# Optimization experiments

Measured on AMD Instinct MI355X. Metric: run time of the kernel, lower is better.

## Reference

```python
import jax, jax.numpy as jnp
import numpy as np

GRID_SIZE = 5
SPLINE_ORDER = 3
B = 524288


def make_grid(in_features, grid_size=GRID_SIZE, spline_order=SPLINE_ORDER, grid_range=(-1.0, 1.0)):
    h = (grid_range[1] - grid_range[0]) / grid_size
    g = jnp.arange(-spline_order, grid_size + spline_order + 1, dtype=jnp.float32) * h + grid_range[0]
    return jnp.tile(g[None, :], (in_features, 1))  # (in, grid_size + 2*order + 1)


def b_splines(x, grid, order=SPLINE_ORDER):
    # x: (B, in), grid: (in, G). Cox-de Boor recursion, matching efficient-kan.
    xe = x[:, :, None]  # (B, in, 1)
    g = grid[None, :, :]  # (1, in, G)
    bases = ((xe >= g[:, :, :-1]) & (xe < g[:, :, 1:])).astype(x.dtype)
    for k in range(1, order + 1):
        left = (xe - g[:, :, : -(k + 1)]) / (g[:, :, k:-1] - g[:, :, : -(k + 1)])
        right = (g[:, :, k + 1:] - xe) / (g[:, :, k + 1:] - g[:, :, 1:-k])
        bases = left * bases[:, :, :-1] + right * bases[:, :, 1:]
    return bases  # (B, in, grid_size + order)


def kan_linear(x, base_w, spline_w, scaler, grid):
    # base path: SiLU activation then dense
    base_out = jax.nn.silu(x) @ base_w.T  # (B, out)
    # spline path
    bs = b_splines(x, grid)  # (B, in, K)
    scaled_sw = spline_w * scaler[:, :, None]  # (out, in, K)
    spline_out = jnp.einsum('bik,oik->bo', bs, scaled_sw)
    return base_out + spline_out


def setup_inputs() -> dict:
    key = jax.random.key(0)
    ks = jax.random.split(key, 7)
    return {
        'x': jax.random.normal(ks[0], (B, 1), dtype=jnp.float32),
        'base_w1': jax.random.normal(ks[1], (8, 1), dtype=jnp.float32) * 0.5,
        'spline_w1': jax.random.normal(ks[2], (8, 1, GRID_SIZE + SPLINE_ORDER), dtype=jnp.float32) * 0.1,
        'scaler1': jax.random.normal(ks[3], (8, 1), dtype=jnp.float32) * 0.5,
        'base_w2': jax.random.normal(ks[4], (1, 8), dtype=jnp.float32) * 0.5,
        'spline_w2': jax.random.normal(ks[5], (1, 8, GRID_SIZE + SPLINE_ORDER), dtype=jnp.float32) * 0.1,
        'scaler2': jax.random.normal(ks[6], (1, 8), dtype=jnp.float32) * 0.5,
    }


def reference(x, base_w1, spline_w1, scaler1, base_w2, spline_w2, scaler2):
    grid1 = make_grid(1)
    grid2 = make_grid(8)
    h = kan_linear(x, base_w1, spline_w1, scaler1, grid1)  # (B, 8)
    out = kan_linear(h, base_w2, spline_w2, scaler2, grid2)  # (B, 1)
    return out
```

## Files before the change

kernel.cpp:

```cpp
#include <hip/hip_runtime.h>


__device__ __forceinline__ float silu_fast(float x) {
    return x * __builtin_amdgcn_rcpf(1.0f + __expf(-x));
}

__global__ __launch_bounds__(256) void kan2_direct(
    const float* __restrict__ bw1, const float* __restrict__ sw1,
    const float* __restrict__ sc1, const float* __restrict__ bw2,
    const float* __restrict__ sw2, const float* __restrict__ sc2,
    const float4* __restrict__ x4, float4* __restrict__ out4, int n4)
{
    __shared__ __align__(16) float w1s[14 * 8];
    __shared__ __align__(16) float w2s[14 * 8];
    const int t = threadIdx.x;
    if (t < 14 * 8) {
        int r = t >> 3, c = t & 7;
        float v1 = 0.0f, v2 = 0.0f;
        if (r >= 3 && r <= 10) {
            int k = r - 3;
            v1 = sw1[c * 8 + k] * sc1[c];
            v2 = sw2[c * 8 + k] * sc2[c];
        }
        w1s[t] = v1;
        w2s[t] = v2;
    }
    __syncthreads();

    float bw1v[8], bw2v[8];
#pragma unroll
    for (int o = 0; o < 8; ++o) { bw1v[o] = bw1[o]; bw2v[o] = bw2[o]; }

    for (int i = blockIdx.x * 256 + t; i < n4; i += gridDim.x * 256) {
        float4 xv = x4[i];
        float vin[4] = {xv.x, xv.y, xv.z, xv.w};
        float vout[4];
#pragma unroll
        for (int cpt = 0; cpt < 4; ++cpt) {
            float x = vin[cpt];

            float s = __fmaf_rn(x, 2.5f, 5.5f);
            s = fminf(fmaxf(s, -20.0f), 40.0f);
            float fc = floorf(s);
            float u  = s - fc;
            int cell = (int)fc;
            float u2 = u * u, u3 = u2 * u;
            float omu = 1.0f - u;
            float n0 = omu * omu * omu * (1.0f / 6.0f);
            float n3 = u3 * (1.0f / 6.0f);
            float n1 = __fmaf_rn(__fmaf_rn(u, 0.5f, -1.0f), u2, 2.0f / 3.0f);
            float n2 = 1.0f - n0 - n1 - n3;
            float nb[4] = {n0, n1, n2, n3};

            float sx = silu_fast(x);
            float h[8];
#pragma unroll
            for (int o = 0; o < 8; ++o) h[o] = sx * bw1v[o];
#pragma unroll
            for (int m = 0; m < 4; ++m) {
                int r = min(max(cell + m, 0), 13);
                const float4 wa = *(const float4*)&w1s[r * 8];
                const float4 wb = *(const float4*)&w1s[r * 8 + 4];
                float bm = nb[m];
                h[0] = __fmaf_rn(bm, wa.x, h[0]);
                h[1] = __fmaf_rn(bm, wa.y, h[1]);
                h[2] = __fmaf_rn(bm, wa.z, h[2]);
                h[3] = __fmaf_rn(bm, wa.w, h[3]);
                h[4] = __fmaf_rn(bm, wb.x, h[4]);
                h[5] = __fmaf_rn(bm, wb.y, h[5]);
                h[6] = __fmaf_rn(bm, wb.z, h[6]);
                h[7] = __fmaf_rn(bm, wb.w, h[7]);
            }

            float acc = 0.0f;
#pragma unroll
            for (int o = 0; o < 8; ++o) {
                float hv = h[o];
                acc = __fmaf_rn(silu_fast(hv), bw2v[o], acc);
                float s2 = __fmaf_rn(hv, 2.5f, 5.5f);
                s2 = fminf(fmaxf(s2, -20.0f), 40.0f);
                float fc2 = floorf(s2);
                float uu  = s2 - fc2;
                int c2 = (int)fc2;
                float uu2 = uu * uu, uu3 = uu2 * uu;
                float womu = 1.0f - uu;
                float q0 = womu * womu * womu * (1.0f / 6.0f);
                float q3 = uu3 * (1.0f / 6.0f);
                float q1 = __fmaf_rn(__fmaf_rn(uu, 0.5f, -1.0f), uu2,
                                     2.0f / 3.0f);
                float q2 = 1.0f - q0 - q1 - q3;
                float qb[4] = {q0, q1, q2, q3};
#pragma unroll
                for (int m = 0; m < 4; ++m) {
                    int r = min(max(c2 + m, 0), 13);
                    acc = __fmaf_rn(qb[m], w2s[r * 8 + o], acc);
                }
            }
            vout[cpt] = acc;
        }
        float4 r4;
        r4.x = vout[0]; r4.y = vout[1]; r4.z = vout[2]; r4.w = vout[3];
        out4[i] = r4;
    }
}

extern "C" void kernel_launch(void* const* d_in, const int* in_sizes, int n_in,
                              void* d_out, int out_size, void* d_ws, size_t ws_size,
                              hipStream_t stream) {
    const float* x   = (const float*)d_in[0];
    const float* bw1 = (const float*)d_in[1];
    const float* sw1 = (const float*)d_in[2];
    const float* sc1 = (const float*)d_in[3];
    const float* bw2 = (const float*)d_in[4];
    const float* sw2 = (const float*)d_in[5];
    const float* sc2 = (const float*)d_in[6];
    float* out = (float*)d_out;
    (void)d_ws; (void)ws_size;

    int n  = in_sizes[0];
    int n4 = n / 4;

    kan2_direct<<<(n4 + 255) / 256, 256, 0, stream>>>(
        bw1, sw1, sc1, bw2, sw2, sc2,
        (const float4*)x, (float4*)out, n4);
}
```

Before: 70.88 us.

## Precompute per-cell cubic polynomial coefficients and evaluate splines via Horner

Each spline cell's four basis weights are folded into per-cell cubic polynomial coefficients in shared memory (float4 per cell/output, padded stride 9), so each spline becomes a single float4 LDS read plus three FMAs, replacing four basis evaluations and four weight loads. It also switches from four elements per thread with float4 I/O to one element per thread with scalar loads, which launches four times as many blocks. The clamping changes from [-20,40] with per-row clamping to clamping s to [0,14), which matches the reference only if out-of-range cells hold zero coefficients. It also changes floating-point rounding slightly.

```diff
diff --git a/kernel.cpp b/kernel.cpp
--- a/kernel.cpp
+++ b/kernel.cpp
@@ -5,25 +5,39 @@
     return x * __builtin_amdgcn_rcpf(1.0f + __expf(-x));
 }
 
-__global__ __launch_bounds__(256) void kan2_direct(
+#define STRIDE 9
+
+__global__ __launch_bounds__(256) void kan2_cell(
     const float* __restrict__ bw1, const float* __restrict__ sw1,
     const float* __restrict__ sc1, const float* __restrict__ bw2,
     const float* __restrict__ sw2, const float* __restrict__ sc2,
-    const float4* __restrict__ x4, float4* __restrict__ out4, int n4)
+    const float* __restrict__ x, float* __restrict__ out, int n)
 {
-    __shared__ __align__(16) float w1s[14 * 8];
-    __shared__ __align__(16) float w2s[14 * 8];
+    __shared__ __align__(16) float4 c1[14 * STRIDE];
+    __shared__ __align__(16) float4 c2[14 * STRIDE];
     const int t = threadIdx.x;
-    if (t < 14 * 8) {
-        int r = t >> 3, c = t & 7;
-        float v1 = 0.0f, v2 = 0.0f;
-        if (r >= 3 && r <= 10) {
-            int k = r - 3;
-            v1 = sw1[c * 8 + k] * sc1[c];
-            v2 = sw2[c * 8 + k] * sc2[c];
+
+    if (t < 112) {
+        int c = t >> 3, o = t & 7;
+        float w1v[4], w2v[4];
+#pragma unroll
+        for (int m = 0; m < 4; ++m) {
+            int k = c - 3 + m;
+            bool in = (k >= 0) && (k <= 7);
+            w1v[m] = in ? sw1[o * 8 + k] * sc1[o] : 0.0f;
+            w2v[m] = in ? sw2[o * 8 + k] * sc2[o] : 0.0f;
         }
-        w1s[t] = v1;
-        w2s[t] = v2;
+        float4 a1, a2;
+        a1.x = (w1v[0] + 4.0f * w1v[1] + w1v[2]) * (1.0f / 6.0f);
+        a1.y = (w1v[2] - w1v[0]) * 0.5f;
+        a1.z = (w1v[0] + w1v[2]) * 0.5f - w1v[1];
+        a1.w = (w1v[3] - w1v[0] + 3.0f * (w1v[1] - w1v[2])) * (1.0f / 6.0f);
+        a2.x = (w2v[0] + 4.0f * w2v[1] + w2v[2]) * (1.0f / 6.0f);
+        a2.y = (w2v[2] - w2v[0]) * 0.5f;
+        a2.z = (w2v[0] + w2v[2]) * 0.5f - w2v[1];
+        a2.w = (w2v[3] - w2v[0] + 3.0f * (w2v[1] - w2v[2])) * (1.0f / 6.0f);
+        c1[c * STRIDE + o] = a1;
+        c2[c * STRIDE + o] = a2;
     }
     __syncthreads();
 
@@ -31,76 +45,40 @@
 #pragma unroll
     for (int o = 0; o < 8; ++o) { bw1v[o] = bw1[o]; bw2v[o] = bw2[o]; }
 
-    for (int i = blockIdx.x * 256 + t; i < n4; i += gridDim.x * 256) {
-        float4 xv = x4[i];
-        float vin[4] = {xv.x, xv.y, xv.z, xv.w};
-        float vout[4];
+    for (int i = blockIdx.x * 256 + t; i < n; i += gridDim.x * 256) {
+        float xv = x[i];
+
+        float s = __fmaf_rn(xv, 2.5f, 5.5f);
+        s = fminf(fmaxf(s, 0.0f), 13.999999f);
+        float fc = floorf(s);
+        int   c  = (int)fc;
+        float u  = s - fc;
+        float sx = silu_fast(xv);
+
+        float h[8];
 #pragma unroll
-        for (int cpt = 0; cpt < 4; ++cpt) {
-            float x = vin[cpt];
+        for (int o = 0; o < 8; ++o) {
+            float4 A = c1[c * STRIDE + o];
+            float p = __fmaf_rn(__fmaf_rn(__fmaf_rn(A.w, u, A.z), u, A.y),
+                                u, A.x);
+            h[o] = __fmaf_rn(sx, bw1v[o], p);
+        }
 
-            float s = __fmaf_rn(x, 2.5f, 5.5f);
-            s = fminf(fmaxf(s, -20.0f), 40.0f);
-            float fc = floorf(s);
-            float u  = s - fc;
-            int cell = (int)fc;
-            float u2 = u * u, u3 = u2 * u;
-            float omu = 1.0f - u;
-            float n0 = omu * omu * omu * (1.0f / 6.0f);
-            float n3 = u3 * (1.0f / 6.0f);
-            float n1 = __fmaf_rn(__fmaf_rn(u, 0.5f, -1.0f), u2, 2.0f / 3.0f);
-            float n2 = 1.0f - n0 - n1 - n3;
-            float nb[4] = {n0, n1, n2, n3};
-
-            float sx = silu_fast(x);
-            float h[8];
+        float acc = 0.0f;
 #pragma unroll
-            for (int o = 0; o < 8; ++o) h[o] = sx * bw1v[o];
-#pragma unroll
-            for (int m = 0; m < 4; ++m) {
-                int r = min(max(cell + m, 0), 13);
-                const float4 wa = *(const float4*)&w1s[r * 8];
-                const float4 wb = *(const float4*)&w1s[r * 8 + 4];
-                float bm = nb[m];
-                h[0] = __fmaf_rn(bm, wa.x, h[0]);
-                h[1] = __fmaf_rn(bm, wa.y, h[1]);
-                h[2] = __fmaf_rn(bm, wa.z, h[2]);
-                h[3] = __fmaf_rn(bm, wa.w, h[3]);
-                h[4] = __fmaf_rn(bm, wb.x, h[4]);
-                h[5] = __fmaf_rn(bm, wb.y, h[5]);
-                h[6] = __fmaf_rn(bm, wb.z, h[6]);
-                h[7] = __fmaf_rn(bm, wb.w, h[7]);
-            }
-
-            float acc = 0.0f;
-#pragma unroll
-            for (int o = 0; o < 8; ++o) {
-                float hv = h[o];
-                acc = __fmaf_rn(silu_fast(hv), bw2v[o], acc);
-                float s2 = __fmaf_rn(hv, 2.5f, 5.5f);
-                s2 = fminf(fmaxf(s2, -20.0f), 40.0f);
-                float fc2 = floorf(s2);
-                float uu  = s2 - fc2;
-                int c2 = (int)fc2;
-                float uu2 = uu * uu, uu3 = uu2 * uu;
-                float womu = 1.0f - uu;
-                float q0 = womu * womu * womu * (1.0f / 6.0f);
-                float q3 = uu3 * (1.0f / 6.0f);
-                float q1 = __fmaf_rn(__fmaf_rn(uu, 0.5f, -1.0f), uu2,
-                                     2.0f / 3.0f);
-                float q2 = 1.0f - q0 - q1 - q3;
-                float qb[4] = {q0, q1, q2, q3};
-#pragma unroll
-                for (int m = 0; m < 4; ++m) {
-                    int r = min(max(c2 + m, 0), 13);
-                    acc = __fmaf_rn(qb[m], w2s[r * 8 + o], acc);
-                }
-            }
-            vout[cpt] = acc;
+        for (int o = 0; o < 8; ++o) {
+            float hv = h[o];
+            float s2 = __fmaf_rn(hv, 2.5f, 5.5f);
+            s2 = fminf(fmaxf(s2, 0.0f), 13.999999f);
+            float fc2 = floorf(s2);
+            int   cc  = (int)fc2;
+            float uu  = s2 - fc2;
+            float4 A = c2[cc * STRIDE + o];
+            float p = __fmaf_rn(__fmaf_rn(__fmaf_rn(A.w, uu, A.z), uu, A.y),
+                                uu, A.x);
+            acc = __fmaf_rn(silu_fast(hv), bw2v[o], acc + p);
         }
-        float4 r4;
-        r4.x = vout[0]; r4.y = vout[1]; r4.z = vout[2]; r4.w = vout[3];
-        out4[i] = r4;
+        out[i] = acc;
     }
 }
 
@@ -117,10 +95,9 @@
     float* out = (float*)d_out;
     (void)d_ws; (void)ws_size;
 
-    int n  = in_sizes[0];
-    int n4 = n / 4;
+    int n = in_sizes[0];
+    int blocks = (n + 255) / 256;
 
-    kan2_direct<<<(n4 + 255) / 256, 256, 0, stream>>>(
-        bw1, sw1, sc1, bw2, sw2, sc2,
-        (const float4*)x, (float4*)out, n4);
+    kan2_cell<<<blocks, 256, 0, stream>>>(
+        bw1, sw1, sc1, bw2, sw2, sc2, x, out, n);
 }
```

New measurement: 69.81 us. No clear change (-1.5%).
